# Kernel tuning notes

Hardware: AMD Instinct MI355X
Metric: run time of the kernel (lower is better)

The kernel has to match this reference:

```python
import jax, jax.numpy as jnp
import numpy as np

DIM = 1024
FF = 4096
BATCH = 4
SEQ = 2048
EPS = 1e-5


def setup_inputs() -> dict:
    key = jax.random.key(0)
    ks = jax.random.split(key, 8)
    x = jax.random.normal(ks[0], (BATCH, SEQ, DIM), dtype=jnp.float32)
    # phazor init: exp(2j*pi*arange(dim)/dim) * |randn(dim)|
    ang = 2.0 * np.pi * jnp.arange(DIM, dtype=jnp.float32) / DIM
    mag = jnp.abs(jax.random.normal(ks[1], (DIM,), dtype=jnp.float32))
    phazor_re = mag * jnp.cos(ang)
    phazor_im = mag * jnp.sin(ang)
    last_re = jax.random.normal(ks[2], (DIM,), dtype=jnp.float32)
    last_im = jax.random.normal(ks[3], (DIM,), dtype=jnp.float32)
    w1 = jax.random.normal(ks[4], (FF, DIM), dtype=jnp.float32) * DIM ** -0.5
    b1 = jnp.zeros((FF,), dtype=jnp.float32)
    w2 = jax.random.normal(ks[5], (DIM, FF), dtype=jnp.float32) * FF ** -0.5
    b2 = jnp.zeros((DIM,), dtype=jnp.float32)
    return {
        'x': x,
        'ln1_w': jnp.ones((DIM,), jnp.float32), 'ln1_b': jnp.zeros((DIM,), jnp.float32),
        'ln2_w': jnp.ones((DIM,), jnp.float32), 'ln2_b': jnp.zeros((DIM,), jnp.float32),
        'sc_lin': jnp.ones((DIM,), jnp.float32),
        'phazor_re': phazor_re, 'phazor_im': phazor_im,
        'last_re': last_re, 'last_im': last_im,
        'w1': w1, 'b1': b1, 'w2': w2, 'b2': b2,
    }


def _layer_norm(x, w, b):
    mu = jnp.mean(x, axis=-1, keepdims=True)
    var = jnp.mean(jnp.square(x - mu), axis=-1, keepdims=True)
    return (x - mu) * jax.lax.rsqrt(var + EPS) * w + b


def _sconv(x, phazor_re, phazor_im, last_re, last_im):
    B, L, D = x.shape
    dtype = x.dtype
    xc = x.astype(jnp.complex64)
    p_raw = phazor_re + 1j * phazor_im
    # tanh(|p|) * exp(i*angle(p))
    p = (jnp.tanh(jnp.abs(p_raw)) * jnp.exp(1j * jnp.angle(p_raw))).astype(jnp.complex64)
    t = jnp.arange(L)[:, None]
    prog = jnp.power(p[None, :], t)            # [L, D] complex
    filt_fft = jnp.fft.fft(prog, n=2 * L, axis=0)   # [2L, D]
    x_fft = jnp.fft.fft(xc, n=2 * L, axis=1)        # [B, 2L, D]
    conv = jnp.fft.ifft(filt_fft[None] * x_fft, axis=1)[:, :L]  # [B, L, D]
    last = (last_re + 1j * last_im)[None, None, :]  # [1,1,D] broadcast over batch
    conv_with_past = conv + last * prog[None] * p[None, None]
    return conv_with_past.real.astype(dtype)


def reference(x, ln1_w, ln1_b, ln2_w, ln2_b, sc_lin,
              phazor_re, phazor_im, last_re, last_im,
              w1, b1, w2, b2):
    # SConv branch
    x_res = x
    h = _layer_norm(x, ln1_w, ln1_b)
    h = jax.nn.silu(h)
    h = _sconv(h, phazor_re, phazor_im, last_re, last_im)
    h = h * sc_lin
    x = h + x_res
    # FFN branch
    x_res = x
    h = _layer_norm(x, ln2_w, ln2_b)
    h = jax.nn.silu(jnp.einsum('bld,fd->blf', h, w1) + b1)
    h = jnp.einsum('blf,df->bld', h, w2) + b2
    return h + x_res
```

## Files before the change

kernel.cpp:

```cpp
#include <hip/hip_runtime.h>
#include <cmath>


#define DIMD 1024
#define FFD  4096
#define BATCH 4
#define SEQL 2048
#define MROWS (BATCH*SEQL)
#define EPSF 1e-5f
#define CHUNKS 32
#define CLEN (SEQL/CHUNKS)

typedef __attribute__((ext_vector_type(8)))  _Float16 half8;
typedef __attribute__((ext_vector_type(4)))  _Float16 half4;
typedef __attribute__((ext_vector_type(4)))  float    floatx4;
typedef __attribute__((ext_vector_type(16))) float    floatx16;

#define ST_OFF   0u
#define E_OFF    33554432u
#define SIN_OFF  34603008u
#define H2_OFF   35651584u
#define W1H_OFF  52428800u
#define W2H_OFF  60817408u
#define Y1_OFF   69206016u

__device__ __forceinline__ void load_lds16(const _Float16* g, _Float16* l) {
    __builtin_amdgcn_global_load_lds(
        (const __attribute__((address_space(1))) unsigned int*)g,
        (__attribute__((address_space(3))) unsigned int*)l,
        16, 0, 0);
}

__global__ __launch_bounds__(256)
void cast_f32_f16(const float* __restrict__ src, _Float16* __restrict__ dst) {
    int i = (blockIdx.x * 256 + threadIdx.x) * 4;
    float4 v = *(const float4*)(src + i);
    half4 o;
    o.x = (_Float16)v.x; o.y = (_Float16)v.y; o.z = (_Float16)v.z; o.w = (_Float16)v.w;
    *(half4*)(dst + i) = o;
}

__global__ __launch_bounds__(256)
void ln_stats(const float* __restrict__ x, float2* __restrict__ st) {
    const size_t row = blockIdx.x;
    const int tid = threadIdx.x;
    float4 v = *(const float4*)(x + row * DIMD + tid * 4);
    float s = (v.x + v.y) + (v.z + v.w);
    float q = (v.x * v.x + v.y * v.y) + (v.z * v.z + v.w * v.w);
    #pragma unroll
    for (int off = 32; off; off >>= 1) {
        s += __shfl_down(s, off, 64);
        q += __shfl_down(q, off, 64);
    }
    __shared__ float red[8];
    if (!(tid & 63)) { red[tid >> 6] = s; red[4 + (tid >> 6)] = q; }
    __syncthreads();
    if (tid == 0) {
        s = (red[0] + red[1]) + (red[2] + red[3]);
        q = (red[4] + red[5]) + (red[6] + red[7]);
        const float mu = s * (1.f / DIMD);
        const float rs = rsqrtf(q * (1.f / DIMD) - mu * mu + EPSF);
        st[row] = make_float2(mu, rs);
    }
}

__global__ __launch_bounds__(256)
void ln_kernel(const float* __restrict__ x, const float* __restrict__ w,
               const float* __restrict__ b, _Float16* __restrict__ oh) {
    const size_t row = blockIdx.x;
    const int tid = threadIdx.x;
    float4 v = *(const float4*)(x + row * DIMD + tid * 4);
    float s = (v.x + v.y) + (v.z + v.w);
    float q = (v.x * v.x + v.y * v.y) + (v.z * v.z + v.w * v.w);
    #pragma unroll
    for (int off = 32; off; off >>= 1) {
        s += __shfl_down(s, off, 64);
        q += __shfl_down(q, off, 64);
    }
    __shared__ float red[8];
    if (!(tid & 63)) { red[tid >> 6] = s; red[4 + (tid >> 6)] = q; }
    __syncthreads();
    s = (red[0] + red[1]) + (red[2] + red[3]);
    q = (red[4] + red[5]) + (red[6] + red[7]);
    const float mu = s * (1.f / DIMD);
    const float rs = rsqrtf(q * (1.f / DIMD) - mu * mu + EPSF);
    float4 wv = *(const float4*)(w + tid * 4);
    float4 bv = *(const float4*)(b + tid * 4);
    half4 hv;
    hv.x = (_Float16)((v.x - mu) * rs * wv.x + bv.x);
    hv.y = (_Float16)((v.y - mu) * rs * wv.y + bv.y);
    hv.z = (_Float16)((v.z - mu) * rs * wv.z + bv.z);
    hv.w = (_Float16)((v.w - mu) * rs * wv.w + bv.w);
    *(half4*)(oh + row * DIMD + tid * 4) = hv;
}

__device__ __forceinline__ void get_p(const float* pre, const float* pim, int d,
                                      float& pr, float& pi) {
    float re = pre[d], im = pim[d];
    float r = sqrtf(re * re + im * im);
    float t = tanhf(r) / fmaxf(r, 1e-30f);
    pr = re * t; pi = im * t;
}

__device__ __forceinline__ float ln_silu(float xv, float2 st, float wd, float bd) {
    float o = (xv - st.x) * st.y * wd + bd;
    return o / (1.f + __expf(-o));
}

__global__ __launch_bounds__(256)
void scan_partial(const float* __restrict__ x, const float2* __restrict__ st,
                  const float* __restrict__ lw, const float* __restrict__ lb,
                  const float* __restrict__ pre, const float* __restrict__ pim,
                  float2* __restrict__ e) {
    const int d = blockIdx.x * 256 + threadIdx.x;
    const int c = blockIdx.y;
    const int bb = blockIdx.z;
    float pr, pi; get_p(pre, pim, d, pr, pi);
    const float wd = lw[d], bd = lb[d];
    float sr = 0.f, si = 0.f;
    const size_t row0 = (size_t)bb * SEQL + (size_t)c * CLEN;
    #pragma unroll 4
    for (int j = 0; j < CLEN; ++j) {
        float xv = x[(row0 + j) * DIMD + d];
        float2 sj = st[row0 + j];
        float hv = ln_silu(xv, sj, wd, bd);
        float nr = pr * sr - pi * si + hv;
        float ni = pr * si + pi * sr;
        sr = nr; si = ni;
    }
    e[((size_t)bb * CHUNKS + c) * DIMD + d] = make_float2(sr, si);
}

__global__ __launch_bounds__(256)
void scan_combine(const float2* __restrict__ e, const float* __restrict__ pre,
                  const float* __restrict__ pim, const float* __restrict__ lre,
                  const float* __restrict__ lim, float2* __restrict__ sv) {
    const int d = blockIdx.x * 256 + threadIdx.x;
    const int bb = blockIdx.y;
    float pr, pi; get_p(pre, pim, d, pr, pi);
    float qr = pr, qi = pi;
    #pragma unroll
    for (int s = 0; s < 6; ++s) {
        float nr = qr * qr - qi * qi;
        float ni = 2.f * qr * qi;
        qr = nr; qi = ni;
    }
    float sr = lre[d], si = lim[d];
    for (int c = 0; c < CHUNKS; ++c) {
        sv[((size_t)bb * CHUNKS + c) * DIMD + d] = make_float2(sr, si);
        float2 ec = e[((size_t)bb * CHUNKS + c) * DIMD + d];
        float nr = qr * sr - qi * si + ec.x;
        float ni = qr * si + qi * sr + ec.y;
        sr = nr; si = ni;
    }
}

__global__ __launch_bounds__(256)
void scan_final(const float* __restrict__ x, const float2* __restrict__ st,
                const float* __restrict__ lw, const float* __restrict__ lb,
                const float* __restrict__ pre, const float* __restrict__ pim,
                const float* __restrict__ sc, const float2* __restrict__ sv,
                float* __restrict__ x2) {
    const int d = blockIdx.x * 256 + threadIdx.x;
    const int c = blockIdx.y;
    const int bb = blockIdx.z;
    float pr, pi; get_p(pre, pim, d, pr, pi);
    const float wd = lw[d], bd = lb[d];
    float2 s0 = sv[((size_t)bb * CHUNKS + c) * DIMD + d];
    float sr = s0.x, si = s0.y;
    const float scd = sc[d];
    const size_t row0 = (size_t)bb * SEQL + (size_t)c * CLEN;
    #pragma unroll 4
    for (int j = 0; j < CLEN; ++j) {
        float xv = x[(row0 + j) * DIMD + d];
        float2 sj = st[row0 + j];
        float hv = ln_silu(xv, sj, wd, bd);
        float nr = pr * sr - pi * si + hv;
        float ni = pr * si + pi * sr;
        sr = nr; si = ni;
        x2[(row0 + j) * DIMD + d] = xv + scd * sr;
    }
}

#define GBM 128
#define GBN 128
#define GBK 64

template<int NCOLS, int EPI>
__global__ __launch_bounds__(256)
void gemm_128(const _Float16* __restrict__ A, const _Float16* __restrict__ W,
              const float* __restrict__ bias, _Float16* __restrict__ out_h,
              const float* __restrict__ resid, float* __restrict__ out_f,
              int N, int K) {
    __shared__ _Float16 As[GBM * GBK];
    __shared__ _Float16 Bs[GBN * GBK];
    const int tid  = threadIdx.x;
    const int lane = tid & 63;
    const int wave = tid >> 6;
    const int wm = (wave >> 1) * 64;
    const int wn = (wave & 1) * 64;
    const int n  = blockIdx.y * gridDim.x + blockIdx.x;
    const int xc = n & 7, ii = n >> 3;
    const size_t m0 = (size_t)(xc + ((ii / NCOLS) << 3)) * GBM;
    const size_t n0 = (size_t)(ii % NCOLS) * GBN;
    const int r32 = lane & 31;
    const int kg  = lane >> 5;

    const int srow = wave * 32 + (lane >> 3);
    const int ccp  = ((lane & 7) ^ (lane >> 3)) * 8;
    const _Float16* ag = A + (m0 + srow) * (size_t)K + ccp;
    const _Float16* wg = W + (n0 + srow) * (size_t)K + ccp;
    _Float16* asl = &As[(wave * 32) * GBK];
    _Float16* bsl = &Bs[(wave * 32) * GBK];

    floatx16 acc[2][2] = {};

    for (int k0 = 0; k0 < K; k0 += GBK) {
        #pragma unroll
        for (int t = 0; t < 4; ++t) {
            load_lds16(ag + k0 + (size_t)(t * 8) * K, asl + t * 8 * GBK);
            load_lds16(wg + k0 + (size_t)(t * 8) * K, bsl + t * 8 * GBK);
        }
        __syncthreads();
        #pragma unroll
        for (int ks = 0; ks < 4; ++ks) {
            const int slot = (((ks << 1) | kg) ^ (r32 & 7)) * 8;
            half8 af0 = *(const half8*)(&As[(wm +      r32) * GBK + slot]);
            half8 af1 = *(const half8*)(&As[(wm + 32 + r32) * GBK + slot]);
            half8 bf0 = *(const half8*)(&Bs[(wn +      r32) * GBK + slot]);
            half8 bf1 = *(const half8*)(&Bs[(wn + 32 + r32) * GBK + slot]);
            acc[0][0] = __builtin_amdgcn_mfma_f32_32x32x16_f16(af0, bf0, acc[0][0], 0, 0, 0);
            acc[0][1] = __builtin_amdgcn_mfma_f32_32x32x16_f16(af0, bf1, acc[0][1], 0, 0, 0);
            acc[1][0] = __builtin_amdgcn_mfma_f32_32x32x16_f16(af1, bf0, acc[1][0], 0, 0, 0);
            acc[1][1] = __builtin_amdgcn_mfma_f32_32x32x16_f16(af1, bf1, acc[1][1], 0, 0, 0);
        }
        __syncthreads();
    }

    #pragma unroll
    for (int ib = 0; ib < 2; ++ib) {
        #pragma unroll
        for (int jb = 0; jb < 2; ++jb) {
            const size_t gn = n0 + wn + jb * 32 + r32;
            const float bb = bias[gn];
            #pragma unroll
            for (int r = 0; r < 16; ++r) {
                const size_t gm = m0 + wm + ib * 32 + (r & 3) + 8 * (r >> 2) + 4 * kg;
                float v = acc[ib][jb][r] + bb;
                if (EPI == 1) {
                    float sl = v / (1.f + __expf(-v));
                    out_h[gm * (size_t)N + gn] = (_Float16)sl;
                } else {
                    out_f[gm * (size_t)N + gn] = v + resid[gm * (size_t)N + gn];
                }
            }
        }
    }
}

extern "C" void kernel_launch(void* const* d_in, const int* in_sizes, int n_in,
                              void* d_out, int out_size, void* d_ws, size_t ws_size,
                              hipStream_t stream) {
    const float* x    = (const float*)d_in[0];
    const float* ln1w = (const float*)d_in[1];
    const float* ln1b = (const float*)d_in[2];
    const float* ln2w = (const float*)d_in[3];
    const float* ln2b = (const float*)d_in[4];
    const float* sc   = (const float*)d_in[5];
    const float* pre  = (const float*)d_in[6];
    const float* pim  = (const float*)d_in[7];
    const float* lre  = (const float*)d_in[8];
    const float* lim  = (const float*)d_in[9];
    const float* w1   = (const float*)d_in[10];
    const float* b1   = (const float*)d_in[11];
    const float* w2   = (const float*)d_in[12];
    const float* b2   = (const float*)d_in[13];

    char* ws = (char*)d_ws;
    float2*     st  = (float2*)(ws + ST_OFF);
    float2*     e   = (float2*)(ws + E_OFF);
    float2*     sv  = (float2*)(ws + SIN_OFF);
    _Float16*   h2  = (_Float16*)(ws + H2_OFF);
    _Float16*   w1h = (_Float16*)(ws + W1H_OFF);
    _Float16*   w2h = (_Float16*)(ws + W2H_OFF);
    _Float16*   y1  = (_Float16*)(ws + Y1_OFF);
    float*      x2  = (float*)d_out;
    float*      outp = (float*)d_out;

    cast_f32_f16<<<dim3(FFD * DIMD / 1024), 256, 0, stream>>>(w1, w1h);
    cast_f32_f16<<<dim3(FFD * DIMD / 1024), 256, 0, stream>>>(w2, w2h);
    ln_stats<<<dim3(MROWS), 256, 0, stream>>>(x, st);
    scan_partial<<<dim3(DIMD / 256, CHUNKS, BATCH), 256, 0, stream>>>(
        x, st, ln1w, ln1b, pre, pim, e);
    scan_combine<<<dim3(DIMD / 256, BATCH), 256, 0, stream>>>(
        e, pre, pim, lre, lim, sv);
    scan_final<<<dim3(DIMD / 256, CHUNKS, BATCH), 256, 0, stream>>>(
        x, st, ln1w, ln1b, pre, pim, sc, sv, x2);
    ln_kernel<<<dim3(MROWS), 256, 0, stream>>>(x2, ln2w, ln2b, h2);
    gemm_128<32, 1><<<dim3(FFD / GBN, MROWS / GBM), 256, 0, stream>>>(
        h2, w1h, b1, y1, nullptr, nullptr, FFD, DIMD);
    gemm_128<8, 2><<<dim3(DIMD / GBN, MROWS / GBM), 256, 0, stream>>>(
        y1, w2h, b2, nullptr, x2, outp, DIMD, FFD);
}
```

Before: 355.5 us.

## Rework chunked scan to 128 chunks with float4 lanes; use 16x16 MFMA for second GEMM

The chunked complex scan now splits the sequence into 128 chunks of 16 rows instead of 32 chunks of 64. Each thread handles four adjacent channels with float4 loads and stores, and the combine step raises p to the 16th power to match the new chunk length. The second GEMM moves to a separate kernel built on 16x16x32 MFMA tiles with a per-lane epilogue, while the first GEMM keeps the 32x32 path. This aims to shorten the serial dependency chain in the scan and improve memory coalescing, at the cost of a longer serial combine loop and more register pressure from the 4x4 accumulator array.

```diff
diff --git a/kernel.cpp b/kernel.cpp
--- a/kernel.cpp
+++ b/kernel.cpp
@@ -8,8 +8,8 @@
 #define SEQL 2048
 #define MROWS (BATCH*SEQL)
 #define EPSF 1e-5f
-#define CHUNKS 32
-#define CLEN (SEQL/CHUNKS)
+#define CHUNKS2 128
+#define CLEN2 (SEQL/CHUNKS2)
 
 typedef __attribute__((ext_vector_type(8)))  _Float16 half8;
 typedef __attribute__((ext_vector_type(4)))  _Float16 half4;
@@ -17,8 +17,8 @@
 typedef __attribute__((ext_vector_type(16))) float    floatx16;
 
 #define ST_OFF   0u
-#define E_OFF    33554432u
-#define SIN_OFF  34603008u
+#define E_OFF    1048576u
+#define SV_OFF   5242880u
 #define H2_OFF   35651584u
 #define W1H_OFF  52428800u
 #define W2H_OFF  60817408u
@@ -102,33 +102,41 @@
     pr = re * t; pi = im * t;
 }
 
-__device__ __forceinline__ float ln_silu(float xv, float2 st, float wd, float bd) {
-    float o = (xv - st.x) * st.y * wd + bd;
-    return o / (1.f + __expf(-o));
-}
-
 __global__ __launch_bounds__(256)
 void scan_partial(const float* __restrict__ x, const float2* __restrict__ st,
                   const float* __restrict__ lw, const float* __restrict__ lb,
                   const float* __restrict__ pre, const float* __restrict__ pim,
                   float2* __restrict__ e) {
-    const int d = blockIdx.x * 256 + threadIdx.x;
-    const int c = blockIdx.y;
-    const int bb = blockIdx.z;
-    float pr, pi; get_p(pre, pim, d, pr, pi);
-    const float wd = lw[d], bd = lb[d];
-    float sr = 0.f, si = 0.f;
-    const size_t row0 = (size_t)bb * SEQL + (size_t)c * CLEN;
-    #pragma unroll 4
-    for (int j = 0; j < CLEN; ++j) {
-        float xv = x[(row0 + j) * DIMD + d];
+    const int tid = threadIdx.x;
+    const int c = blockIdx.x;
+    const int bb = blockIdx.y;
+    const int d0 = tid * 4;
+    float pr[4], pi[4];
+    #pragma unroll
+    for (int k = 0; k < 4; ++k) get_p(pre, pim, d0 + k, pr[k], pi[k]);
+    const float4 wv = *(const float4*)(lw + d0);
+    const float4 bv = *(const float4*)(lb + d0);
+    const float wa[4] = {wv.x, wv.y, wv.z, wv.w};
+    const float ba[4] = {bv.x, bv.y, bv.z, bv.w};
+    const size_t row0 = (size_t)bb * SEQL + (size_t)c * CLEN2;
+    float sr[4] = {0.f, 0.f, 0.f, 0.f}, si[4] = {0.f, 0.f, 0.f, 0.f};
+    #pragma unroll
+    for (int j = 0; j < CLEN2; ++j) {
+        float4 v = *(const float4*)(x + (row0 + j) * DIMD + d0);
         float2 sj = st[row0 + j];
-        float hv = ln_silu(xv, sj, wd, bd);
-        float nr = pr * sr - pi * si + hv;
-        float ni = pr * si + pi * sr;
-        sr = nr; si = ni;
-    }
-    e[((size_t)bb * CHUNKS + c) * DIMD + d] = make_float2(sr, si);
+        const float xa[4] = {v.x, v.y, v.z, v.w};
+        #pragma unroll
+        for (int k = 0; k < 4; ++k) {
+            float o = (xa[k] - sj.x) * sj.y * wa[k] + ba[k];
+            float h = o / (1.f + __expf(-o));
+            float nr = pr[k] * sr[k] - pi[k] * si[k] + h;
+            float ni = pr[k] * si[k] + pi[k] * sr[k];
+            sr[k] = nr; si[k] = ni;
+        }
+    }
+    float2* ep = e + ((size_t)bb * CHUNKS2 + c) * DIMD + d0;
+    #pragma unroll
+    for (int k = 0; k < 4; ++k) ep[k] = make_float2(sr[k], si[k]);
 }
 
 __global__ __launch_bounds__(256)
@@ -140,15 +148,15 @@
     float pr, pi; get_p(pre, pim, d, pr, pi);
     float qr = pr, qi = pi;
     #pragma unroll
-    for (int s = 0; s < 6; ++s) {
+    for (int s = 0; s < 4; ++s) {
         float nr = qr * qr - qi * qi;
         float ni = 2.f * qr * qi;
         qr = nr; qi = ni;
     }
     float sr = lre[d], si = lim[d];
-    for (int c = 0; c < CHUNKS; ++c) {
-        sv[((size_t)bb * CHUNKS + c) * DIMD + d] = make_float2(sr, si);
-        float2 ec = e[((size_t)bb * CHUNKS + c) * DIMD + d];
+    for (int c = 0; c < CHUNKS2; ++c) {
+        sv[((size_t)bb * CHUNKS2 + c) * DIMD + d] = make_float2(sr, si);
+        float2 ec = e[((size_t)bb * CHUNKS2 + c) * DIMD + d];
         float nr = qr * sr - qi * si + ec.x;
         float ni = qr * si + qi * sr + ec.y;
         sr = nr; si = ni;
@@ -161,24 +169,43 @@
                 const float* __restrict__ pre, const float* __restrict__ pim,
                 const float* __restrict__ sc, const float2* __restrict__ sv,
                 float* __restrict__ x2) {
-    const int d = blockIdx.x * 256 + threadIdx.x;
-    const int c = blockIdx.y;
-    const int bb = blockIdx.z;
-    float pr, pi; get_p(pre, pim, d, pr, pi);
-    const float wd = lw[d], bd = lb[d];
-    float2 s0 = sv[((size_t)bb * CHUNKS + c) * DIMD + d];
-    float sr = s0.x, si = s0.y;
-    const float scd = sc[d];
-    const size_t row0 = (size_t)bb * SEQL + (size_t)c * CLEN;
-    #pragma unroll 4
-    for (int j = 0; j < CLEN; ++j) {
-        float xv = x[(row0 + j) * DIMD + d];
+    const int tid = threadIdx.x;
+    const int c = blockIdx.x;
+    const int bb = blockIdx.y;
+    const int d0 = tid * 4;
+    float pr[4], pi[4];
+    #pragma unroll
+    for (int k = 0; k < 4; ++k) get_p(pre, pim, d0 + k, pr[k], pi[k]);
+    const float4 wv = *(const float4*)(lw + d0);
+    const float4 bv = *(const float4*)(lb + d0);
+    const float4 scv = *(const float4*)(sc + d0);
+    const float wa[4] = {wv.x, wv.y, wv.z, wv.w};
+    const float ba[4] = {bv.x, bv.y, bv.z, bv.w};
+    const float sca[4] = {scv.x, scv.y, scv.z, scv.w};
+    const size_t row0 = (size_t)bb * SEQL + (size_t)c * CLEN2;
+    float sr[4], si[4];
+    {
+        const float2* s0 = sv + ((size_t)bb * CHUNKS2 + c) * DIMD + d0;
+        #pragma unroll
+        for (int k = 0; k < 4; ++k) { sr[k] = s0[k].x; si[k] = s0[k].y; }
+    }
+    #pragma unroll
+    for (int j = 0; j < CLEN2; ++j) {
+        float4 v = *(const float4*)(x + (row0 + j) * DIMD + d0);
         float2 sj = st[row0 + j];
-        float hv = ln_silu(xv, sj, wd, bd);
-        float nr = pr * sr - pi * si + hv;
-        float ni = pr * si + pi * sr;
-        sr = nr; si = ni;
-        x2[(row0 + j) * DIMD + d] = xv + scd * sr;
+        const float xa[4] = {v.x, v.y, v.z, v.w};
+        float out[4];
+        #pragma unroll
+        for (int k = 0; k < 4; ++k) {
+            float o = (xa[k] - sj.x) * sj.y * wa[k] + ba[k];
+            float h = o / (1.f + __expf(-o));
+            float nr = pr[k] * sr[k] - pi[k] * si[k] + h;
+            float ni = pr[k] * si[k] + pi[k] * sr[k];
+            sr[k] = nr; si[k] = ni;
+            out[k] = xa[k] + sca[k] * nr;
+        }
+        float4 ov = {out[0], out[1], out[2], out[3]};
+        *(float4*)(x2 + (row0 + j) * DIMD + d0) = ov;
     }
 }
 
@@ -186,11 +213,10 @@
 #define GBN 128
 #define GBK 64
 
-template<int NCOLS, int EPI>
-__global__ __launch_bounds__(256)
-void gemm_128(const _Float16* __restrict__ A, const _Float16* __restrict__ W,
+template<int NCOLS>
+__global__ __launch_bounds__(256)
+void gemm1_32(const _Float16* __restrict__ A, const _Float16* __restrict__ W,
               const float* __restrict__ bias, _Float16* __restrict__ out_h,
-              const float* __restrict__ resid, float* __restrict__ out_f,
               int N, int K) {
     __shared__ _Float16 As[GBM * GBK];
     __shared__ _Float16 Bs[GBN * GBK];
@@ -247,12 +273,77 @@
             for (int r = 0; r < 16; ++r) {
                 const size_t gm = m0 + wm + ib * 32 + (r & 3) + 8 * (r >> 2) + 4 * kg;
                 float v = acc[ib][jb][r] + bb;
-                if (EPI == 1) {
-                    float sl = v / (1.f + __expf(-v));
-                    out_h[gm * (size_t)N + gn] = (_Float16)sl;
-                } else {
-                    out_f[gm * (size_t)N + gn] = v + resid[gm * (size_t)N + gn];
-                }
+                float sl = v / (1.f + __expf(-v));
+                out_h[gm * (size_t)N + gn] = (_Float16)sl;
+            }
+        }
+    }
+}
+
+template<int NCOLS>
+__global__ __launch_bounds__(256)
+void gemm2_16(const _Float16* __restrict__ A, const _Float16* __restrict__ W,
+              const float* __restrict__ bias, const float* __restrict__ resid,
+              float* __restrict__ out_f, int N, int K) {
+    __shared__ _Float16 As[GBM * GBK];
+    __shared__ _Float16 Bs[GBN * GBK];
+    const int tid  = threadIdx.x;
+    const int lane = tid & 63;
+    const int wave = tid >> 6;
+    const int wm = (wave >> 1) * 64;
+    const int wn = (wave & 1) * 64;
+    const int n  = blockIdx.y * gridDim.x + blockIdx.x;
+    const int xc = n & 7, ii = n >> 3;
+    const size_t m0 = (size_t)(xc + ((ii / NCOLS) << 3)) * GBM;
+    const size_t n0 = (size_t)(ii % NCOLS) * GBN;
+    const int fr = lane & 15;
+    const int quad = lane >> 4;
+
+    const int srow = wave * 32 + (lane >> 3);
+    const int ccp  = ((lane & 7) ^ (lane >> 3)) * 8;
+    const _Float16* ag = A + (m0 + srow) * (size_t)K + ccp;
+    const _Float16* wg = W + (n0 + srow) * (size_t)K + ccp;
+    _Float16* asl = &As[(wave * 32) * GBK];
+    _Float16* bsl = &Bs[(wave * 32) * GBK];
+
+    floatx4 acc[4][4] = {};
+
+    for (int k0 = 0; k0 < K; k0 += GBK) {
+        #pragma unroll
+        for (int t = 0; t < 4; ++t) {
+            load_lds16(ag + k0 + (size_t)(t * 8) * K, asl + t * 8 * GBK);
+            load_lds16(wg + k0 + (size_t)(t * 8) * K, bsl + t * 8 * GBK);
+        }
+        __syncthreads();
+        #pragma unroll
+        for (int kk = 0; kk < GBK; kk += 32) {
+            half8 af[4], bf[4];
+            #pragma unroll
+            for (int i = 0; i < 4; ++i) {
+                const int slot = (((kk >> 3) + quad) ^ (fr & 7)) * 8;
+                af[i] = *(const half8*)(&As[(wm + i * 16 + fr) * GBK + slot]);
+                bf[i] = *(const half8*)(&Bs[(wn + i * 16 + fr) * GBK + slot]);
+            }
+            #pragma unroll
+            for (int i = 0; i < 4; ++i)
+                #pragma unroll
+                for (int j = 0; j < 4; ++j)
+                    acc[i][j] = __builtin_amdgcn_mfma_f32_16x16x32_f16(
+                        af[i], bf[j], acc[i][j], 0, 0, 0);
+        }
+        __syncthreads();
+    }
+
+    #pragma unroll
+    for (int i = 0; i < 4; ++i) {
+        #pragma unroll
+        for (int j = 0; j < 4; ++j) {
+            #pragma unroll
+            for (int r = 0; r < 4; ++r) {
+                const size_t gm = m0 + wm + i * 16 + quad * 4 + r;
+                const size_t gn = n0 + wn + j * 16 + fr;
+                float v = acc[i][j][r] + bias[gn];
+                out_f[gm * (size_t)N + gn] = v + resid[gm * (size_t)N + gn];
             }
         }
     }
@@ -279,7 +370,7 @@
     char* ws = (char*)d_ws;
     float2*     st  = (float2*)(ws + ST_OFF);
     float2*     e   = (float2*)(ws + E_OFF);
-    float2*     sv  = (float2*)(ws + SIN_OFF);
+    float2*     sv  = (float2*)(ws + SV_OFF);
     _Float16*   h2  = (_Float16*)(ws + H2_OFF);
     _Float16*   w1h = (_Float16*)(ws + W1H_OFF);
     _Float16*   w2h = (_Float16*)(ws + W2H_OFF);
@@ -290,15 +381,15 @@
     cast_f32_f16<<<dim3(FFD * DIMD / 1024), 256, 0, stream>>>(w1, w1h);
     cast_f32_f16<<<dim3(FFD * DIMD / 1024), 256, 0, stream>>>(w2, w2h);
     ln_stats<<<dim3(MROWS), 256, 0, stream>>>(x, st);
-    scan_partial<<<dim3(DIMD / 256, CHUNKS, BATCH), 256, 0, stream>>>(
+    scan_partial<<<dim3(CHUNKS2, BATCH), 256, 0, stream>>>(
         x, st, ln1w, ln1b, pre, pim, e);
     scan_combine<<<dim3(DIMD / 256, BATCH), 256, 0, stream>>>(
         e, pre, pim, lre, lim, sv);
-    scan_final<<<dim3(DIMD / 256, CHUNKS, BATCH), 256, 0, stream>>>(
+    scan_final<<<dim3(CHUNKS2, BATCH), 256, 0, stream>>>(
         x, st, ln1w, ln1b, pre, pim, sc, sv, x2);
     ln_kernel<<<dim3(MROWS), 256, 0, stream>>>(x2, ln2w, ln2b, h2);
-    gemm_128<32, 1><<<dim3(FFD / GBN, MROWS / GBM), 256, 0, stream>>>(
-        h2, w1h, b1, y1, nullptr, nullptr, FFD, DIMD);
-    gemm_128<8, 2><<<dim3(DIMD / GBN, MROWS / GBM), 256, 0, stream>>>(
-        y1, w2h, b2, nullptr, x2, outp, DIMD, FFD);
-}
+    gemm1_32<32><<<dim3(FFD / GBN, MROWS / GBM), 256, 0, stream>>>(
+        h2, w1h, b1, y1, FFD, DIMD);
+    gemm2_16<8><<<dim3(DIMD / GBN, MROWS / GBM), 256, 0, stream>>>(
+        y1, w2h, b2, x2, outp, DIMD, FFD);
+}
```

Measured after the change: 361.9 us. No clear change (+1.8%).
